# Kernel tuning notes

Measured on AMD Instinct MI355X. Metric: run time of the kernel, lower is better.

## Reference

```python
import jax, jax.numpy as jnp
import numpy as np

NUM_HEADS = 32
NUM_KV_HEADS = 8
HEAD_DIM = 128
HIDDEN = 4096
ROPE_THETA = 10000.0
SLIDING_WINDOW = 1024
NEG_INF = -1e9


def _make_sliding_window_mask(q_len, kv_len, window):
    # additive mask: 0 where attendable (causal AND within window), -inf otherwise
    i = jnp.arange(q_len)[:, None]
    j = jnp.arange(kv_len)[None, :]
    allowed = (j <= i) & (j > i - window)
    return jnp.where(allowed, 0.0, NEG_INF).astype(jnp.float32)[None, None]  # [1,1,q,kv]


def _rope_tables(seq_len, head_dim, theta):
    inv_freq = 1.0 / (theta ** (jnp.arange(0, head_dim, 2, dtype=jnp.float32) / head_dim))
    t = jnp.arange(seq_len, dtype=jnp.float32)
    freqs = jnp.einsum('i,j->ij', t, inv_freq)        # [S, D/2]
    emb = jnp.concatenate([freqs, freqs], axis=-1)     # [S, D]
    return jnp.cos(emb), jnp.sin(emb)


def _rotate_half(x):
    d = x.shape[-1] // 2
    return jnp.concatenate([-x[..., d:], x[..., :d]], axis=-1)


def setup_inputs() -> dict:
    key = jax.random.key(0)
    ks = jax.random.split(key, 5)
    B, S = 1, 2048
    sc = 0.02
    hidden_states = jax.random.normal(ks[0], (B, S, HIDDEN), dtype=jnp.float32)
    Wq = jax.random.normal(ks[1], (HIDDEN, NUM_HEADS * HEAD_DIM), dtype=jnp.float32) * sc
    Wk = jax.random.normal(ks[2], (HIDDEN, NUM_KV_HEADS * HEAD_DIM), dtype=jnp.float32) * sc
    Wv = jax.random.normal(ks[3], (HIDDEN, NUM_KV_HEADS * HEAD_DIM), dtype=jnp.float32) * sc
    Wo = jax.random.normal(ks[4], (NUM_HEADS * HEAD_DIM, HIDDEN), dtype=jnp.float32) * sc
    attention_mask = _make_sliding_window_mask(S, S, SLIDING_WINDOW)
    position_ids = jnp.arange(S, dtype=jnp.int64)[None, :]
    return {"hidden_states": hidden_states, "attention_mask": attention_mask,
            "position_ids": position_ids, "Wq": Wq, "Wk": Wk, "Wv": Wv, "Wo": Wo}


def reference(hidden_states, attention_mask, position_ids, Wq, Wk, Wv, Wo):
    B, S, _ = hidden_states.shape
    # projections
    q = (hidden_states @ Wq).reshape(B, S, NUM_HEADS, HEAD_DIM).transpose(0, 2, 1, 3)      # [B,H,S,D]
    k = (hidden_states @ Wk).reshape(B, S, NUM_KV_HEADS, HEAD_DIM).transpose(0, 2, 1, 3)   # [B,Hk,S,D]
    v = (hidden_states @ Wv).reshape(B, S, NUM_KV_HEADS, HEAD_DIM).transpose(0, 2, 1, 3)
    # RoPE
    cos_t, sin_t = _rope_tables(S, HEAD_DIM, ROPE_THETA)
    cos = cos_t[position_ids][:, None]  # [B,1,S,D]
    sin = sin_t[position_ids][:, None]
    q = q * cos + _rotate_half(q) * sin
    k = k * cos + _rotate_half(k) * sin
    # repeat_kv (GQA): [B,Hk,S,D] -> [B,H,S,D]
    n_rep = NUM_HEADS // NUM_KV_HEADS
    k = jnp.repeat(k, n_rep, axis=1)
    v = jnp.repeat(v, n_rep, axis=1)
    # attention
    scores = jnp.einsum('bhqd,bhkd->bhqk', q, k) / np.sqrt(HEAD_DIM)
    scores = scores + attention_mask
    probs = jax.nn.softmax(scores, axis=-1)
    out = jnp.einsum('bhqk,bhkd->bhqd', probs, v)
    out = out.transpose(0, 2, 1, 3).reshape(B, S, HIDDEN)
    return out @ Wo
```

## Files before the change

kernel.cpp:

```cpp
#include <hip/hip_runtime.h>

typedef __attribute__((ext_vector_type(8))) short short8;
typedef __attribute__((ext_vector_type(4))) short s16x4;
typedef __attribute__((ext_vector_type(4))) float f32x4;
typedef unsigned short u16;
typedef unsigned int u32;

__device__ __forceinline__ u16 f2bf(float f) {
  union { float f; unsigned int u; } v; v.f = f;
  unsigned int r = (v.u + 0x7FFFu + ((v.u >> 16) & 1u)) >> 16;
  return (u16)r;
}
__device__ __forceinline__ float bf2f(u16 b) {
  union { unsigned int u; float f; } v; v.u = ((unsigned int)b) << 16;
  return v.f;
}
__device__ __forceinline__ void load_lds16(const void* g, void* l) {
  __builtin_amdgcn_global_load_lds((const __attribute__((address_space(1))) void*)g,
                                   (__attribute__((address_space(3))) void*)l, 16, 0, 0);
}

__global__ void cvt_f32_bf16_kernel(const float* __restrict__ in, u16* __restrict__ out, int n4) {
  int i = blockIdx.x * blockDim.x + threadIdx.x;
  if (i >= n4) return;
  float4 v = ((const float4*)in)[i];
  ushort4 o;
  o.x = f2bf(v.x); o.y = f2bf(v.y); o.z = f2bf(v.z); o.w = f2bf(v.w);
  ((ushort4*)out)[i] = o;
}

__device__ __forceinline__ void tconv64_tile(const float* __restrict__ W, u16* __restrict__ Wt,
                                             int K, int N, int nb, int kb, int tid) {
  __shared__ float tile[64][65];
  int tx = tid & 15, ty = tid >> 4;
  const float* src = W + (size_t)(kb + ty) * N + nb + tx * 4;
#pragma unroll
  for (int i = 0; i < 4; ++i) {
    float4 v = *(const float4*)(src + (size_t)i * 16 * N);
    tile[ty + i * 16][tx * 4 + 0] = v.x;
    tile[ty + i * 16][tx * 4 + 1] = v.y;
    tile[ty + i * 16][tx * 4 + 2] = v.z;
    tile[ty + i * 16][tx * 4 + 3] = v.w;
  }
  __syncthreads();
  u16* dst = Wt + (size_t)(nb + ty) * K + kb + tx * 4;
#pragma unroll
  for (int i = 0; i < 4; ++i) {
    s16x4 o;
#pragma unroll
    for (int j = 0; j < 4; ++j) o[j] = (short)f2bf(tile[tx * 4 + j][ty + i * 16]);
    *(s16x4*)(dst + (size_t)i * 16 * K) = o;
  }
}

__global__ void tconv3_kernel(const float* __restrict__ Wq, const float* __restrict__ Wk,
                              const float* __restrict__ Wv, u16* __restrict__ WqT,
                              u16* __restrict__ WkvT) {
  int id = blockIdx.x;
  if (id < 4096)      tconv64_tile(Wq, WqT, 4096, 4096, (id & 63) * 64, (id >> 6) * 64, threadIdx.x);
  else if (id < 5120) { int t = id - 4096; tconv64_tile(Wk, WkvT, 4096, 1024, (t & 15) * 64, (t >> 4) * 64, threadIdx.x); }
  else                { int t = id - 5120; tconv64_tile(Wv, WkvT + (size_t)1024 * 4096, 4096, 1024, (t & 15) * 64, (t >> 4) * 64, threadIdx.x); }
}

__global__ void tconv1_kernel(const float* __restrict__ W, u16* __restrict__ Wt) {
  int id = blockIdx.x;
  tconv64_tile(W, Wt, 4096, 4096, (id & 63) * 64, (id >> 6) * 64, threadIdx.x);
}

__global__ void t_bf16_kernel(const u16* __restrict__ V, u16* __restrict__ Vt, int ldv, int R, int C) {
  __shared__ u16 tile[32][33];
  int tx = threadIdx.x, ty = threadIdx.y;
  int cb = blockIdx.x * 32, rb = blockIdx.y * 32;
#pragma unroll
  for (int i = ty; i < 32; i += 8)
    tile[i][tx] = V[(size_t)(rb + i) * ldv + cb + tx];
  __syncthreads();
#pragma unroll
  for (int i = ty; i < 32; i += 8)
    Vt[(size_t)(cb + i) * R + rb + tx] = tile[tx][i];
}

__global__ void rope_kernel(u16* __restrict__ Qb, u16* __restrict__ KVb) {
  int idx = blockIdx.x * blockDim.x + threadIdx.x;
  u16* X; int ld, hmask, hshift, id; float scale;
  if (idx < 4194304) { X = Qb;  ld = 4096; hmask = 31; hshift = 5; id = idx;          scale = 0.12751781828987514f; }
  else               { X = KVb; ld = 2048; hmask = 7;  hshift = 3; id = idx - 4194304; scale = 1.0f; }
  int j = id & 63;
  int t = id >> 6;
  int hh = t & hmask;
  int s = t >> hshift;
  float invf = exp2f(-(float)j * (13.287712379549449f / 64.0f));
  float ang = (float)s * invf;
  float sn, cs;
  sincosf(ang, &sn, &cs);
  u16* p = X + (size_t)s * ld + hh * 128 + j;
  float a = bf2f(p[0]), b = bf2f(p[64]);
  p[0]  = f2bf((a * cs - b * sn) * scale);
  p[64] = f2bf((b * cs + a * sn) * scale);
}

template<int OUTF32>
__global__ __launch_bounds__(256, 2) void gemm_bt_kernel(
    const u16* __restrict__ A, const u16* __restrict__ B,
    void* __restrict__ C, int M, int N, int K) {
  __shared__ u16 As[2][128 * 64];
  __shared__ u16 Bs[2][128 * 64];
  int tid = threadIdx.x, lane = tid & 63, w = tid >> 6;
  int wr = w >> 1, wc = w & 1;
  int g = lane >> 4, q = lane & 15;
  int nbx = gridDim.x;
  int flat = blockIdx.y * nbx + blockIdx.x;
  int cpx = (nbx * gridDim.y) >> 3;
  flat = (flat & 7) * cpx + (flat >> 3);
  int m0 = (flat / nbx) * 128, n0 = (flat % nbx) * 128;
  f32x4 acc[4][4];
#pragma unroll
  for (int i = 0; i < 4; ++i)
#pragma unroll
    for (int j = 0; j < 4; ++j) acc[i][j] = (f32x4){0.f, 0.f, 0.f, 0.f};
  int srow = tid >> 3;
  int scol = ((tid & 7) ^ (srow & 7)) << 3;
  const u16* ga = A + (size_t)(m0 + srow) * K + scol;
  const u16* gb = B + (size_t)(n0 + srow) * K + scol;
  int xorm = (q & 7) << 3;
  int arow = wr * 64 + q;
  int brow = wc * 64 + q;
  int nt = K >> 6;

  auto stage = [&](int buf, int t) {
    const u16* pa = ga + t * 64;
    const u16* pb = gb + t * 64;
#pragma unroll
    for (int it = 0; it < 4; ++it) {
      load_lds16(pa + (size_t)it * 32 * K, (char*)(&As[buf][0]) + (it * 256 + w * 64) * 16);
      load_lds16(pb + (size_t)it * 32 * K, (char*)(&Bs[buf][0]) + (it * 256 + w * 64) * 16);
    }
  };

  stage(0, 0);
  stage(1, 1);
  asm volatile("s_waitcnt vmcnt(8)" ::: "memory");
  __builtin_amdgcn_s_barrier();
  for (int t = 0; t < nt; ++t) {
    int cur = t & 1;
    short8 af[2][4], bfr[2][4];
#pragma unroll
    for (int kb = 0; kb < 2; ++kb) {
      int col = (kb * 32 + g * 8) ^ xorm;
#pragma unroll
      for (int m = 0; m < 4; ++m) af[kb][m]  = *(const short8*)&As[cur][(arow + m * 16) * 64 + col];
#pragma unroll
      for (int n = 0; n < 4; ++n) bfr[kb][n] = *(const short8*)&Bs[cur][(brow + n * 16) * 64 + col];
    }
    asm volatile("s_waitcnt lgkmcnt(0)" ::: "memory");
    __builtin_amdgcn_s_barrier();
    if (t + 2 < nt) stage(cur, t + 2);
    __builtin_amdgcn_sched_barrier(0);
    __builtin_amdgcn_s_setprio(1);
#pragma unroll
    for (int kb = 0; kb < 2; ++kb)
#pragma unroll
      for (int m = 0; m < 4; ++m)
#pragma unroll
        for (int n = 0; n < 4; ++n)
          acc[m][n] = __builtin_amdgcn_mfma_f32_16x16x32_bf16(af[kb][m], bfr[kb][n], acc[m][n], 0, 0, 0);
    __builtin_amdgcn_s_setprio(0);
    if (t + 2 < nt)      { asm volatile("s_waitcnt vmcnt(8)" ::: "memory"); }
    else if (t + 1 < nt) { asm volatile("s_waitcnt vmcnt(0)" ::: "memory"); }
    __builtin_amdgcn_s_barrier();
  }
  int crow = m0 + wr * 64 + g * 4;
  int ccol = n0 + wc * 64 + q;
#pragma unroll
  for (int m = 0; m < 4; ++m)
#pragma unroll
    for (int n = 0; n < 4; ++n)
#pragma unroll
      for (int r = 0; r < 4; ++r) {
        size_t off = (size_t)(crow + m * 16 + r) * N + ccol + n * 16;
        if (OUTF32) ((float*)C)[off] = acc[m][n][r];
        else        ((u16*)C)[off]   = f2bf(acc[m][n][r]);
      }
}

template<int OUTF32>
__global__ __launch_bounds__(512, 2) void gemm_wide_kernel(
    const u16* __restrict__ A, const u16* __restrict__ B,
    void* __restrict__ C, int N, int K) {
  __shared__ u16 As[2][128 * 64];
  __shared__ u16 Bs[2][256 * 64];
  int tid = threadIdx.x, lane = tid & 63, wid = tid >> 6;
  int wr = wid >> 2, wc = wid & 3;
  int g = lane >> 4, q = lane & 15;
  int nbx = gridDim.x;
  int id = blockIdx.y * nbx + blockIdx.x;
  int cpx = (nbx * gridDim.y) >> 3;
  int swz = (id & 7) * cpx + (id >> 3);
  int m0 = (swz / nbx) * 128, n0 = (swz % nbx) * 256;
  f32x4 acc[4][4];
#pragma unroll
  for (int i = 0; i < 4; ++i)
#pragma unroll
    for (int j = 0; j < 4; ++j) acc[i][j] = (f32x4){0.f, 0.f, 0.f, 0.f};
  int srow = tid >> 3;
  int scol = ((tid & 7) ^ (srow & 7)) << 3;
  const u16* ga = A + (size_t)(m0 + srow) * K + scol;
  const u16* gb = B + (size_t)(n0 + srow) * K + scol;
  int xorm = (q & 7) << 3;
  int nt = K >> 6;

  auto stage = [&](int buf, int t) {
    const u16* pa = ga + t * 64;
    const u16* pb = gb + t * 64;
#pragma unroll
    for (int it = 0; it < 2; ++it)
      load_lds16(pa + (size_t)it * 64 * K, (char*)(&As[buf][0]) + it * 8192 + tid * 16);
#pragma unroll
    for (int it = 0; it < 4; ++it)
      load_lds16(pb + (size_t)it * 64 * K, (char*)(&Bs[buf][0]) + it * 8192 + tid * 16);
  };

  stage(0, 0);
  stage(1, 1);
  asm volatile("s_waitcnt vmcnt(6)" ::: "memory");
  __builtin_amdgcn_s_barrier();
  for (int t = 0; t < nt; ++t) {
    int cur = t & 1;
    short8 av[2][4], bv[2][4];
#pragma unroll
    for (int kb = 0; kb < 2; ++kb) {
      int col = (kb * 32 + g * 8) ^ xorm;
#pragma unroll
      for (int fm = 0; fm < 4; ++fm)
        av[kb][fm] = *(const short8*)&As[cur][(wr * 64 + fm * 16 + q) * 64 + col];
#pragma unroll
      for (int fn = 0; fn < 4; ++fn)
        bv[kb][fn] = *(const short8*)&Bs[cur][(wc * 64 + fn * 16 + q) * 64 + col];
    }
    asm volatile("s_waitcnt lgkmcnt(0)" ::: "memory");
    __builtin_amdgcn_s_barrier();
    if (t + 2 < nt) stage(cur, t + 2);
    __builtin_amdgcn_sched_barrier(0);
    __builtin_amdgcn_s_setprio(1);
#pragma unroll
    for (int kb = 0; kb < 2; ++kb)
#pragma unroll
      for (int fm = 0; fm < 4; ++fm)
#pragma unroll
        for (int fn = 0; fn < 4; ++fn)
          acc[fm][fn] = __builtin_amdgcn_mfma_f32_16x16x32_bf16(av[kb][fm], bv[kb][fn], acc[fm][fn], 0, 0, 0);
    __builtin_amdgcn_s_setprio(0);
    if (t + 2 < nt)      { asm volatile("s_waitcnt vmcnt(6)" ::: "memory"); }
    else if (t + 1 < nt) { asm volatile("s_waitcnt vmcnt(0)" ::: "memory"); }
    __builtin_amdgcn_s_barrier();
  }
  int crow = m0 + wr * 64 + g * 4;
  int ccol = n0 + wc * 64 + q;
#pragma unroll
  for (int fm = 0; fm < 4; ++fm)
#pragma unroll
    for (int fn = 0; fn < 4; ++fn)
#pragma unroll
      for (int r = 0; r < 4; ++r) {
        size_t off = (size_t)(crow + fm * 16 + r) * N + ccol + fn * 16;
        if (OUTF32) ((float*)C)[off] = acc[fm][fn][r];
        else        ((u16*)C)[off]   = f2bf(acc[fm][fn][r]);
      }
}

__global__ __launch_bounds__(256, 2) void attn_kernel(
    const u16* __restrict__ Q, const u16* __restrict__ Kg,
    const u16* __restrict__ Vt, u16* __restrict__ O) {
  __shared__ u16 Ks[2][64 * 128];
  __shared__ u16 Vs[2][128 * 64];
  int tid = threadIdx.x, lane = tid & 63, w = tid >> 6;
  int g = lane >> 4, q = lane & 15;
  int q0 = blockIdx.x * 64;
  int h = blockIdx.y, hk = h >> 2;
  int qrow = q0 + w * 16;
  int xorm = (lane & 7) << 3;
  short8 qf[4];
  {
    const u16* qp = Q + (size_t)(qrow + q) * 4096 + h * 128 + g * 8;
#pragma unroll
    for (int kk = 0; kk < 4; ++kk) qf[kk] = *(const short8*)(qp + kk * 32);
  }
  float mrow = -1e30f, lsum = 0.f;
  f32x4 of[8];
#pragma unroll
  for (int d = 0; d < 8; ++d) of[d] = (f32x4){0.f, 0.f, 0.f, 0.f};
  int jt_lo = (q0 >= 1024) ? ((q0 - 1023) >> 6) : 0;
  int jt_hi = q0 >> 6;
  int krow = tid >> 4;
  int kchunk = (tid & 15) ^ (krow & 7);
  const u16* kbase = Kg + (size_t)krow * 2048 + hk * 128 + (kchunk << 3);
  int vrow = tid >> 3;
  int vchunk = (tid & 7) ^ (vrow & 7);
  const u16* vbase = Vt + (size_t)(hk * 128 + vrow) * 2048 + (vchunk << 3);

  auto stageK = [&](int buf, int j0) {
    const u16* gp = kbase + (size_t)j0 * 2048;
#pragma unroll
    for (int it = 0; it < 4; ++it)
      load_lds16(gp + (size_t)it * 16 * 2048, (char*)(&Ks[buf][0]) + (it * 256 + w * 64) * 16);
  };
  auto stageV = [&](int buf, int j0) {
    const u16* gp = vbase + j0;
#pragma unroll
    for (int it = 0; it < 4; ++it)
      load_lds16(gp + (size_t)it * 32 * 2048, (char*)(&Vs[buf][0]) + (it * 256 + w * 64) * 16);
  };

  int cur = 0;
  stageK(0, jt_lo << 6);
  stageV(0, jt_lo << 6);
  asm volatile("s_waitcnt vmcnt(0)" ::: "memory");
  __syncthreads();
  for (int jt = jt_lo; jt <= jt_hi; ++jt) {
    int j0 = jt << 6;
    if (jt < jt_hi) { stageK(cur ^ 1, j0 + 64); stageV(cur ^ 1, j0 + 64); }
    f32x4 sf[4];
#pragma unroll
    for (int nt = 0; nt < 4; ++nt) sf[nt] = (f32x4){0.f, 0.f, 0.f, 0.f};
    const u16* ks = &Ks[cur][0];
    __builtin_amdgcn_s_setprio(1);
#pragma unroll
    for (int kk = 0; kk < 4; ++kk) {
      short8 qv = qf[kk];
      int col = (kk * 32 + g * 8) ^ xorm;
#pragma unroll
      for (int nt = 0; nt < 4; ++nt) {
        short8 kf = *(const short8*)&ks[(nt * 16 + q) * 128 + col];
        sf[nt] = __builtin_amdgcn_mfma_f32_16x16x32_bf16(kf, qv, sf[nt], 0, 0, 0);
      }
    }
    __builtin_amdgcn_s_setprio(0);
    float p[4][4];
#pragma unroll
    for (int nt = 0; nt < 4; ++nt)
#pragma unroll
      for (int r = 0; r < 4; ++r) p[nt][r] = sf[nt][r];
    if (j0 + 63 > qrow || j0 + 1009 <= qrow) {
      int qq = qrow + q;
      int kb = j0 + g * 4;
#pragma unroll
      for (int nt = 0; nt < 4; ++nt)
#pragma unroll
        for (int r = 0; r < 4; ++r) {
          int key = kb + nt * 16 + r;
          if (key > qq || key + 1024 <= qq) p[nt][r] = -1e9f;
        }
    }
    float tm = p[0][0];
#pragma unroll
    for (int nt = 0; nt < 4; ++nt)
#pragma unroll
      for (int r = 0; r < 4; ++r) tm = fmaxf(tm, p[nt][r]);
    tm = fmaxf(tm, __shfl_xor(tm, 16));
    tm = fmaxf(tm, __shfl_xor(tm, 32));
    if (__any(tm > mrow + 8.f)) {
      float nm = fmaxf(mrow, tm);
      float sc = __builtin_amdgcn_exp2f(mrow - nm);
      mrow = nm;
      lsum *= sc;
#pragma unroll
      for (int d = 0; d < 8; ++d) of[d] *= sc;
    }
    float ps = 0.f;
#pragma unroll
    for (int nt = 0; nt < 4; ++nt)
#pragma unroll
      for (int r = 0; r < 4; ++r) {
        float e = __builtin_amdgcn_exp2f(p[nt][r] - mrow);
        p[nt][r] = e;
        ps += e;
      }
    ps += __shfl_xor(ps, 16);
    ps += __shfl_xor(ps, 32);
    lsum += ps;
    u32 pk[4][2];
#pragma unroll
    for (int nt = 0; nt < 4; ++nt) {
      pk[nt][0] = __builtin_amdgcn_perm(__float_as_uint(p[nt][1]), __float_as_uint(p[nt][0]), 0x07060302u);
      pk[nt][1] = __builtin_amdgcn_perm(__float_as_uint(p[nt][3]), __float_as_uint(p[nt][2]), 0x07060302u);
    }
    int s0 = q + ((g & 1) ? 32 : 0);
    int s1 = s0 + 16;
    bool hi_sel = g >= 2;
    const u16* vs = &Vs[cur][0];
    __builtin_amdgcn_s_setprio(1);
#pragma unroll
    for (int kh = 0; kh < 2; ++kh) {
      int lo = kh * 2, hi = lo + 1;
      u32 a0 = (u32)__shfl((int)pk[lo][0], s0);
      u32 a1 = (u32)__shfl((int)pk[lo][1], s0);
      u32 b0 = (u32)__shfl((int)pk[hi][0], s0);
      u32 b1 = (u32)__shfl((int)pk[hi][1], s0);
      u32 a2 = (u32)__shfl((int)pk[lo][0], s1);
      u32 a3 = (u32)__shfl((int)pk[lo][1], s1);
      u32 b2 = (u32)__shfl((int)pk[hi][0], s1);
      u32 b3 = (u32)__shfl((int)pk[hi][1], s1);
      union { u32 u[4]; short8 s; } pb;
      pb.u[0] = hi_sel ? b0 : a0;
      pb.u[1] = hi_sel ? b1 : a1;
      pb.u[2] = hi_sel ? b2 : a2;
      pb.u[3] = hi_sel ? b3 : a3;
      int col = (kh * 32 + g * 8) ^ xorm;
#pragma unroll
      for (int dt = 0; dt < 8; ++dt) {
        short8 vv = *(const short8*)&vs[(dt * 16 + q) * 64 + col];
        of[dt] = __builtin_amdgcn_mfma_f32_16x16x32_bf16(vv, pb.s, of[dt], 0, 0, 0);
      }
    }
    __builtin_amdgcn_s_setprio(0);
    asm volatile("s_waitcnt vmcnt(0)" ::: "memory");
    __builtin_amdgcn_s_barrier();
    cur ^= 1;
  }
  float inv = 1.f / lsum;
  u16* op = O + (size_t)(qrow + q) * 4096 + h * 128 + g * 4;
#pragma unroll
  for (int dt = 0; dt < 8; ++dt) {
    s16x4 o4;
#pragma unroll
    for (int r = 0; r < 4; ++r) o4[r] = (short)f2bf(of[dt][r] * inv);
    *(s16x4*)(op + dt * 16) = o4;
  }
}

extern "C" void kernel_launch(void* const* d_in, const int* in_sizes, int n_in,
                              void* d_out, int out_size, void* d_ws, size_t ws_size,
                              hipStream_t stream) {
  (void)in_sizes; (void)n_in; (void)out_size;
  const float* hs = (const float*)d_in[0];
  const float* Wq = (const float*)d_in[3];
  const float* Wk = (const float*)d_in[4];
  const float* Wv = (const float*)d_in[5];
  const float* Wo = (const float*)d_in[6];
  float* out = (float*)d_out;
  char* ws = (char*)d_ws;

  u16* Xb   = (u16*)(ws + 0);
  u16* Wt   = (u16*)(ws + 16777216);
  u16* WkvT = (u16*)(ws + 50331648);
  u16* Qb   = (u16*)(ws + 67108864);
  u16* KVb  = (u16*)(ws + 83886080);
  u16* Vtb  = (u16*)(ws + 92274688);
  u16* Ab   = (u16*)(ws + 96468992);
  if (ws_size < 113246208u) return;

  cvt_f32_bf16_kernel<<<dim3(2097152 / 256), 256, 0, stream>>>(hs, Xb, 2097152);

  tconv3_kernel<<<dim3(6144), 256, 0, stream>>>(Wq, Wk, Wv, Wt, WkvT);

  gemm_wide_kernel<0><<<dim3(16, 16), 512, 0, stream>>>(Xb, Wt, Qb, 4096, 4096);

  gemm_bt_kernel<0><<<dim3(16, 16), 256, 0, stream>>>(Xb, WkvT, KVb, 2048, 2048, 4096);

  rope_kernel<<<dim3(20480), 256, 0, stream>>>(Qb, KVb);

  t_bf16_kernel<<<dim3(32, 64), dim3(32, 8), 0, stream>>>(KVb + 1024, Vtb, 2048, 2048, 1024);

  attn_kernel<<<dim3(32, 32), 256, 0, stream>>>(Qb, KVb, Vtb, Ab);

  tconv1_kernel<<<dim3(4096), 256, 0, stream>>>(Wo, Wt);
  gemm_wide_kernel<1><<<dim3(16, 16), 512, 0, stream>>>(Ab, Wt, out, 4096, 4096);
}
```

Measured before the change: 343.8 us.

## Double-buffer register fragments to overlap LDS reads with MFMA in GEMMs

Restructures both GEMM main loops into a two-step unrolled ping-pong. The next tile's LDS fragments are read into a second register set while the MFMAs for the current tile run. This is meant to hide LDS read latency behind matrix math. In exchange it doubles fragment register usage, which could cause spills or lower occupancy under the launch bounds, and it assumes an even number of K tiles.

```diff
diff --git a/kernel.cpp b/kernel.cpp
--- a/kernel.cpp
+++ b/kernel.cpp
@@ -136,38 +136,59 @@
       load_lds16(pb + (size_t)it * 32 * K, (char*)(&Bs[buf][0]) + (it * 256 + w * 64) * 16);
     }
   };
-
+  auto readFrags = [&](int cur, short8 (&af)[2][4], short8 (&bfr)[2][4]) {
+#pragma unroll
+    for (int kb = 0; kb < 2; ++kb) {
+      int col = (kb * 32 + g * 8) ^ xorm;
+#pragma unroll
+      for (int m = 0; m < 4; ++m) af[kb][m]  = *(const short8*)&As[cur][(arow + m * 16) * 64 + col];
+#pragma unroll
+      for (int n = 0; n < 4; ++n) bfr[kb][n] = *(const short8*)&Bs[cur][(brow + n * 16) * 64 + col];
+    }
+  };
+  auto domfma = [&](short8 (&af)[2][4], short8 (&bfr)[2][4]) {
+    __builtin_amdgcn_s_setprio(1);
+#pragma unroll
+    for (int kb = 0; kb < 2; ++kb)
+#pragma unroll
+      for (int m = 0; m < 4; ++m)
+#pragma unroll
+        for (int n = 0; n < 4; ++n)
+          acc[m][n] = __builtin_amdgcn_mfma_f32_16x16x32_bf16(af[kb][m], bfr[kb][n], acc[m][n], 0, 0, 0);
+    __builtin_amdgcn_s_setprio(0);
+  };
+
+  short8 avA[2][4], bvA[2][4], avB[2][4], bvB[2][4];
   stage(0, 0);
   stage(1, 1);
   asm volatile("s_waitcnt vmcnt(8)" ::: "memory");
   __builtin_amdgcn_s_barrier();
-  for (int t = 0; t < nt; ++t) {
-    int cur = t & 1;
-    short8 af[2][4], bfr[2][4];
-#pragma unroll
-    for (int kb = 0; kb < 2; ++kb) {
-      int col = (kb * 32 + g * 8) ^ xorm;
-#pragma unroll
-      for (int m = 0; m < 4; ++m) af[kb][m]  = *(const short8*)&As[cur][(arow + m * 16) * 64 + col];
-#pragma unroll
-      for (int n = 0; n < 4; ++n) bfr[kb][n] = *(const short8*)&Bs[cur][(brow + n * 16) * 64 + col];
-    }
+  readFrags(0, avA, bvA);
+  for (int t = 0; t < nt; t += 2) {
     asm volatile("s_waitcnt lgkmcnt(0)" ::: "memory");
     __builtin_amdgcn_s_barrier();
-    if (t + 2 < nt) stage(cur, t + 2);
+    if (t + 2 < nt) {
+      stage(0, t + 2);
+      asm volatile("s_waitcnt vmcnt(8)" ::: "memory");
+    } else {
+      asm volatile("s_waitcnt vmcnt(0)" ::: "memory");
+    }
+    __builtin_amdgcn_s_barrier();
+    readFrags(1, avB, bvB);
     __builtin_amdgcn_sched_barrier(0);
-    __builtin_amdgcn_s_setprio(1);
-#pragma unroll
-    for (int kb = 0; kb < 2; ++kb)
-#pragma unroll
-      for (int m = 0; m < 4; ++m)
-#pragma unroll
-        for (int n = 0; n < 4; ++n)
-          acc[m][n] = __builtin_amdgcn_mfma_f32_16x16x32_bf16(af[kb][m], bfr[kb][n], acc[m][n], 0, 0, 0);
-    __builtin_amdgcn_s_setprio(0);
-    if (t + 2 < nt)      { asm volatile("s_waitcnt vmcnt(8)" ::: "memory"); }
-    else if (t + 1 < nt) { asm volatile("s_waitcnt vmcnt(0)" ::: "memory"); }
-    __builtin_amdgcn_s_barrier();
+    domfma(avA, bvA);
+    asm volatile("s_waitcnt lgkmcnt(0)" ::: "memory");
+    __builtin_amdgcn_s_barrier();
+    if (t + 3 < nt) {
+      stage(1, t + 3);
+      asm volatile("s_waitcnt vmcnt(8)" ::: "memory");
+    } else {
+      asm volatile("s_waitcnt vmcnt(0)" ::: "memory");
+    }
+    __builtin_amdgcn_s_barrier();
+    if (t + 2 < nt) readFrags(0, avA, bvA);
+    __builtin_amdgcn_sched_barrier(0);
+    domfma(avB, bvB);
   }
   int crow = m0 + wr * 64 + g * 4;
   int ccol = n0 + wc * 64 + q;
@@ -219,40 +240,61 @@
     for (int it = 0; it < 4; ++it)
       load_lds16(pb + (size_t)it * 64 * K, (char*)(&Bs[buf][0]) + it * 8192 + tid * 16);
   };
-
+  auto readFrags = [&](int cur, short8 (&av)[2][4], short8 (&bv)[2][4]) {
+#pragma unroll
+    for (int kb = 0; kb < 2; ++kb) {
+      int col = (kb * 32 + g * 8) ^ xorm;
+#pragma unroll
+      for (int fm = 0; fm < 4; ++fm)
+        av[kb][fm] = *(const short8*)&As[cur][(wr * 64 + fm * 16 + q) * 64 + col];
+#pragma unroll
+      for (int fn = 0; fn < 4; ++fn)
+        bv[kb][fn] = *(const short8*)&Bs[cur][(wc * 64 + fn * 16 + q) * 64 + col];
+    }
+  };
+  auto domfma = [&](short8 (&av)[2][4], short8 (&bv)[2][4]) {
+    __builtin_amdgcn_s_setprio(1);
+#pragma unroll
+    for (int kb = 0; kb < 2; ++kb)
+#pragma unroll
+      for (int fm = 0; fm < 4; ++fm)
+#pragma unroll
+        for (int fn = 0; fn < 4; ++fn)
+          acc[fm][fn] = __builtin_amdgcn_mfma_f32_16x16x32_bf16(av[kb][fm], bv[kb][fn], acc[fm][fn], 0, 0, 0);
+    __builtin_amdgcn_s_setprio(0);
+  };
+
+  short8 avA[2][4], bvA[2][4], avB[2][4], bvB[2][4];
   stage(0, 0);
   stage(1, 1);
   asm volatile("s_waitcnt vmcnt(6)" ::: "memory");
   __builtin_amdgcn_s_barrier();
-  for (int t = 0; t < nt; ++t) {
-    int cur = t & 1;
-    short8 av[2][4], bv[2][4];
-#pragma unroll
-    for (int kb = 0; kb < 2; ++kb) {
-      int col = (kb * 32 + g * 8) ^ xorm;
-#pragma unroll
-      for (int fm = 0; fm < 4; ++fm)
-        av[kb][fm] = *(const short8*)&As[cur][(wr * 64 + fm * 16 + q) * 64 + col];
-#pragma unroll
-      for (int fn = 0; fn < 4; ++fn)
-        bv[kb][fn] = *(const short8*)&Bs[cur][(wc * 64 + fn * 16 + q) * 64 + col];
-    }
+  readFrags(0, avA, bvA);
+  for (int t = 0; t < nt; t += 2) {
     asm volatile("s_waitcnt lgkmcnt(0)" ::: "memory");
     __builtin_amdgcn_s_barrier();
-    if (t + 2 < nt) stage(cur, t + 2);
+    if (t + 2 < nt) {
+      stage(0, t + 2);
+      asm volatile("s_waitcnt vmcnt(6)" ::: "memory");
+    } else {
+      asm volatile("s_waitcnt vmcnt(0)" ::: "memory");
+    }
+    __builtin_amdgcn_s_barrier();
+    readFrags(1, avB, bvB);
     __builtin_amdgcn_sched_barrier(0);
-    __builtin_amdgcn_s_setprio(1);
-#pragma unroll
-    for (int kb = 0; kb < 2; ++kb)
-#pragma unroll
-      for (int fm = 0; fm < 4; ++fm)
-#pragma unroll
-        for (int fn = 0; fn < 4; ++fn)
-          acc[fm][fn] = __builtin_amdgcn_mfma_f32_16x16x32_bf16(av[kb][fm], bv[kb][fn], acc[fm][fn], 0, 0, 0);
-    __builtin_amdgcn_s_setprio(0);
-    if (t + 2 < nt)      { asm volatile("s_waitcnt vmcnt(6)" ::: "memory"); }
-    else if (t + 1 < nt) { asm volatile("s_waitcnt vmcnt(0)" ::: "memory"); }
-    __builtin_amdgcn_s_barrier();
+    domfma(avA, bvA);
+    asm volatile("s_waitcnt lgkmcnt(0)" ::: "memory");
+    __builtin_amdgcn_s_barrier();
+    if (t + 3 < nt) {
+      stage(1, t + 3);
+      asm volatile("s_waitcnt vmcnt(6)" ::: "memory");
+    } else {
+      asm volatile("s_waitcnt vmcnt(0)" ::: "memory");
+    }
+    __builtin_amdgcn_s_barrier();
+    if (t + 2 < nt) readFrags(0, avA, bvA);
+    __builtin_amdgcn_sched_barrier(0);
+    domfma(avB, bvB);
   }
   int crow = m0 + wr * 64 + g * 4;
   int ccol = n0 + wc * 64 + q;
```

Measured after the change: 484.3 us. +40.9%, slower.
